# Kernel optimization log

Measured on AMD Instinct MI355X. Metric: run time of the kernel, lower is better.

The kernel has to match this reference:

```python
import jax, jax.numpy as jnp
import numpy as np

IN_DIM = 18 * 2 * 1 * 536  # 19296
H = 512
OUT = 11
STEPS = 1024


def setup_inputs() -> dict:
    key = jax.random.key(0)
    ks = jax.random.split(key, 14)
    s = 0.02  # small init scale for stable LSTM dynamics
    f32 = jnp.float32
    return {
        "inputs": jax.random.normal(ks[0], (STEPS, IN_DIM), dtype=f32),
        "W_in": jax.random.normal(ks[1], (H, IN_DIM), dtype=f32) * s,
        "b_in": jnp.zeros((H,), dtype=f32),
        "Wih0": jax.random.normal(ks[2], (4 * H, H), dtype=f32) * s,
        "Whh0": jax.random.normal(ks[3], (4 * H, H), dtype=f32) * s,
        "bih0": jnp.zeros((4 * H,), dtype=f32),
        "bhh0": jnp.zeros((4 * H,), dtype=f32),
        "Wih1": jax.random.normal(ks[4], (4 * H, H), dtype=f32) * s,
        "Whh1": jax.random.normal(ks[5], (4 * H, H), dtype=f32) * s,
        "bih1": jnp.zeros((4 * H,), dtype=f32),
        "bhh1": jnp.zeros((4 * H,), dtype=f32),
        "W_out": jax.random.normal(ks[6], (OUT, H), dtype=f32) * s,
        "b_out": jnp.zeros((OUT,), dtype=f32),
    }


def _lstm_cell(gates, c):
    # PyTorch gate order: input, forget, cell(g), output
    i, f, g, o = jnp.split(gates, 4, axis=-1)
    c_new = jax.nn.sigmoid(f) * c + jax.nn.sigmoid(i) * jnp.tanh(g)
    h_new = jax.nn.sigmoid(o) * jnp.tanh(c_new)
    return h_new, c_new


def reference(inputs, W_in, b_in, Wih0, Whh0, bih0, bhh0,
              Wih1, Whh1, bih1, bhh1, W_out, b_out):
    # Input projection is time-independent -> batch it across all steps.
    x_proj = inputs @ W_in.T + b_in            # (STEPS, H)
    gx0 = x_proj @ Wih0.T + bih0               # (STEPS, 4H) precomputed layer-0 input gates

    def step(carry, gx0_t):
        h0, c0, h1, c1 = carry
        h0, c0 = _lstm_cell(gx0_t + h0 @ Whh0.T + bhh0, c0)
        h1, c1 = _lstm_cell(h0 @ Wih1.T + bih1 + h1 @ Whh1.T + bhh1, c1)
        return (h0, c0, h1, c1), h1

    z = jnp.zeros((H,), dtype=inputs.dtype)
    (h0, c0, h1, c1), hs = jax.lax.scan(step, (z, z, z, z), gx0)
    outputs = (hs @ W_out.T + b_out)[:, None, :]   # (STEPS, 1, OUT) == torch (steps, batch=1, 11)
    hn = jnp.stack([h0, h1])[:, None, :]           # (num_layers=2, batch=1, H)
    cn = jnp.stack([c0, c1])[:, None, :]
    return outputs, hn, cn
```

## Files before the change

kernel.cpp:

```cpp
#include <hip/hip_runtime.h>
#include <math.h>

typedef unsigned long long ull;
typedef unsigned int u32;
typedef unsigned short u16;
typedef _Float16 half2v __attribute__((ext_vector_type(2)));
typedef __bf16 bf16x8 __attribute__((ext_vector_type(8)));
typedef float f32x4 __attribute__((ext_vector_type(4)));

#define H 512
#define STEPS 1024
#define OUTN 11

__device__ __forceinline__ float sigm(float x) { return 1.f / (1.f + __expf(-x)); }
__device__ __forceinline__ ull ld_pair(const ull* p) {
  return __hip_atomic_load((ull*)p, __ATOMIC_RELAXED, __HIP_MEMORY_SCOPE_AGENT);
}
__device__ __forceinline__ void st_pair(ull* p, ull v) {
  __hip_atomic_store(p, v, __ATOMIC_RELAXED, __HIP_MEMORY_SCOPE_AGENT);
}
__device__ __forceinline__ float dot2acc(half2v a, half2v b, float c) {
#if __has_builtin(__builtin_amdgcn_fdot2)
  return __builtin_amdgcn_fdot2(a, b, c, false);
#else
  return c + (float)a.x * (float)b.x + (float)a.y * (float)b.y;
#endif
}
__device__ __forceinline__ u16 f16bits(float x) {
  return __builtin_bit_cast(u16, (_Float16)x);
}
__device__ __forceinline__ half2v bch2(u32 u) { return __builtin_bit_cast(half2v, u); }

__device__ __forceinline__ u32 split_bf16(float x) {
  u32 u = __float_as_uint(x);
  u32 rh = (u + 0x7FFFu + ((u >> 16) & 1u)) & 0xFFFF0000u;
  float hf = __uint_as_float(rh);
  float lo = x - hf;
  u32 ul = __float_as_uint(lo);
  u32 rl = (ul + 0x7FFFu + ((ul >> 16) & 1u)) & 0xFFFF0000u;
  return (rh >> 16) | rl;
}

__global__ void cvt_split(float* __restrict__ A, float* __restrict__ B, int nA, int n4) {
  int idx = blockIdx.x * 256 + threadIdx.x;
  if (idx >= n4) return;
  int base = idx * 4;
  float* p = (base < nA) ? (A + base) : (B + (base - nA));
  float4 v = *(float4*)p;
  u32 r0 = split_bf16(v.x), r1 = split_bf16(v.y), r2 = split_bf16(v.z), r3 = split_bf16(v.w);
  uint4 o = make_uint4(r0, r1, r2, r3);
  *(uint4*)p = o;
}

__global__ __launch_bounds__(256, 2)
void gemm_hilo(const u32* __restrict__ A2, const u32* __restrict__ B2,
               float* __restrict__ C, int M, int N, int K)
{
  __shared__ __align__(16) u16 Ah[64 * 32], Al[64 * 32], Bh[64 * 32], Bl[64 * 32];
  const int z = blockIdx.z;
  const int zstart = z * 151;
  const int nsteps = (z < 3) ? 151 : 150;
  const int mt = blockIdx.x * 64, nt = blockIdx.y * 64;
  const int tid = threadIdx.x;
  const int row = tid >> 2, cg = (tid & 3) * 8;
  const int wave = tid >> 6, lane = tid & 63;
  const int wm = (wave & 1) * 32, wn = (wave >> 1) * 32;
  const int quad = lane >> 4, l16 = lane & 15;

  f32x4 acc[2][2];
#pragma unroll
  for (int i = 0; i < 2; ++i)
#pragma unroll
    for (int j = 0; j < 2; ++j) acc[i][j] = (f32x4)0.f;

  for (int s = 0; s < nsteps; ++s) {
    const int kb = (zstart + s) * 32;
    {
      const u32* ap = A2 + (size_t)(mt + row) * K + kb + cg;
      const u32* bp = B2 + (size_t)(nt + row) * K + kb + cg;
      uint4 a0 = *(const uint4*)ap, a1 = *(const uint4*)(ap + 4);
      uint4 b0 = *(const uint4*)bp, b1 = *(const uint4*)(bp + 4);
      uint4 hi, lo;
      hi = make_uint4((a0.x & 0xFFFF) | (a0.y << 16), (a0.z & 0xFFFF) | (a0.w << 16),
                      (a1.x & 0xFFFF) | (a1.y << 16), (a1.z & 0xFFFF) | (a1.w << 16));
      lo = make_uint4((a0.x >> 16) | (a0.y & 0xFFFF0000u), (a0.z >> 16) | (a0.w & 0xFFFF0000u),
                      (a1.x >> 16) | (a1.y & 0xFFFF0000u), (a1.z >> 16) | (a1.w & 0xFFFF0000u));
      *(uint4*)&Ah[row * 32 + cg] = hi;
      *(uint4*)&Al[row * 32 + cg] = lo;
      hi = make_uint4((b0.x & 0xFFFF) | (b0.y << 16), (b0.z & 0xFFFF) | (b0.w << 16),
                      (b1.x & 0xFFFF) | (b1.y << 16), (b1.z & 0xFFFF) | (b1.w << 16));
      lo = make_uint4((b0.x >> 16) | (b0.y & 0xFFFF0000u), (b0.z >> 16) | (b0.w & 0xFFFF0000u),
                      (b1.x >> 16) | (b1.y & 0xFFFF0000u), (b1.z >> 16) | (b1.w & 0xFFFF0000u));
      *(uint4*)&Bh[row * 32 + cg] = hi;
      *(uint4*)&Bl[row * 32 + cg] = lo;
    }
    __syncthreads();
    bf16x8 ah[2], al[2], bh[2], bl[2];
#pragma unroll
    for (int mf = 0; mf < 2; ++mf) {
      int r = (wm + mf * 16 + l16) * 32 + quad * 8;
      ah[mf] = *reinterpret_cast<const bf16x8*>(&Ah[r]);
      al[mf] = *reinterpret_cast<const bf16x8*>(&Al[r]);
    }
#pragma unroll
    for (int nf = 0; nf < 2; ++nf) {
      int r = (wn + nf * 16 + l16) * 32 + quad * 8;
      bh[nf] = *reinterpret_cast<const bf16x8*>(&Bh[r]);
      bl[nf] = *reinterpret_cast<const bf16x8*>(&Bl[r]);
    }
#pragma unroll
    for (int mf = 0; mf < 2; ++mf)
#pragma unroll
      for (int nf = 0; nf < 2; ++nf) {
        acc[mf][nf] = __builtin_amdgcn_mfma_f32_16x16x32_bf16(ah[mf], bh[nf], acc[mf][nf], 0, 0, 0);
        acc[mf][nf] = __builtin_amdgcn_mfma_f32_16x16x32_bf16(ah[mf], bl[nf], acc[mf][nf], 0, 0, 0);
        acc[mf][nf] = __builtin_amdgcn_mfma_f32_16x16x32_bf16(al[mf], bh[nf], acc[mf][nf], 0, 0, 0);
      }
    __syncthreads();
  }

#pragma unroll
  for (int mf = 0; mf < 2; ++mf)
#pragma unroll
    for (int nf = 0; nf < 2; ++nf)
#pragma unroll
      for (int r = 0; r < 4; ++r) {
        int rw = mt + wm + mf * 16 + quad * 4 + r;
        int cl = nt + wn + nf * 16 + l16;
        atomicAdd(&C[(size_t)rw * N + cl], acc[mf][nf][r]);
      }
}

#define GBM 64
#define GBN 64
#define GBK 64
#define GLD 76

__global__ __launch_bounds__(256, 2)
void gemm_nt(const float* __restrict__ A, const float* __restrict__ B,
             float* __restrict__ C, const float* __restrict__ bias,
             int M, int N, int K)
{
  __shared__ float As[GBM][GLD];
  __shared__ float Bs[GBN][GLD];
  const int mt = blockIdx.x, nt = blockIdx.y;
  const int tid = threadIdx.x;
  const int tx = tid & 15, ty = tid >> 4;

  float acc[4][4] = {{0.f}};

  for (int kb = 0; kb < K; kb += GBK) {
#pragma unroll
    for (int i = 0; i < 4; ++i) {
      int r = ty + i * 16;
      int gk = kb + tx * 4;
      *(float4*)&As[r][tx * 4] = *(const float4*)(A + (size_t)(mt * GBM + r) * K + gk);
      *(float4*)&Bs[r][tx * 4] = *(const float4*)(B + (size_t)(nt * GBN + r) * K + gk);
    }
    __syncthreads();
#pragma unroll
    for (int k4 = 0; k4 < GBK; k4 += 4) {
      float4 a[4], b[4];
#pragma unroll
      for (int i = 0; i < 4; ++i) a[i] = *(const float4*)&As[ty * 4 + i][k4];
#pragma unroll
      for (int j = 0; j < 4; ++j) b[j] = *(const float4*)&Bs[tx * 4 + j][k4];
#pragma unroll
      for (int i = 0; i < 4; ++i)
#pragma unroll
        for (int j = 0; j < 4; ++j) {
          acc[i][j] = fmaf(a[i].x, b[j].x, acc[i][j]);
          acc[i][j] = fmaf(a[i].y, b[j].y, acc[i][j]);
          acc[i][j] = fmaf(a[i].z, b[j].z, acc[i][j]);
          acc[i][j] = fmaf(a[i].w, b[j].w, acc[i][j]);
        }
    }
    __syncthreads();
  }

#pragma unroll
  for (int i = 0; i < 4; ++i) {
    int m = mt * GBM + ty * 4 + i;
#pragma unroll
    for (int j = 0; j < 4; ++j) {
      int n = nt * GBN + tx * 4 + j;
      C[(size_t)m * N + n] = acc[i][j] + bias[n];
    }
  }
}

__global__ void init_xproj(float* __restrict__ xp, const float* __restrict__ b_in) {
  int i = blockIdx.x * 256 + threadIdx.x;
  xp[i] = b_in[i & (H - 1)];
}

__global__ void out_proj(const float* __restrict__ hs1, const float* __restrict__ Wout,
                         const float* __restrict__ bout, float* __restrict__ out) {
  int idx = blockIdx.x * 256 + threadIdx.x;
  if (idx >= STEPS * OUTN) return;
  int t = idx / OUTN, o = idx - t * OUTN;
  const float* h = hs1 + t * H;
  const float* wr = Wout + o * H;
  float acc = 0.f;
#pragma unroll 4
  for (int i = 0; i < H; i += 4) {
    float4 hv = *(const float4*)(h + i);
    float4 wv = *(const float4*)(wr + i);
    acc = fmaf(hv.x, wv.x, acc);
    acc = fmaf(hv.y, wv.y, acc);
    acc = fmaf(hv.z, wv.z, acc);
    acc = fmaf(hv.w, wv.w, acc);
  }
  out[idx] = acc + bout[o];
}

#define NC0 24
#define NC1 16
#define RD 8

__global__ __launch_bounds__(512, 1)
void lstm_chains(const float* __restrict__ gx0,
                 const float* __restrict__ Whh0, const float* __restrict__ bhh0,
                 const float* __restrict__ Wih1, const float* __restrict__ Whh1,
                 const float* __restrict__ bih1, const float* __restrict__ bhh1,
                 float* __restrict__ hs1, float* __restrict__ out,
                 ull* __restrict__ mb0, ull* __restrict__ mb1,
                 int* __restrict__ flags1)
{
  const int wg = blockIdx.x;
  const int tid = threadIdx.x;
  const bool role0 = (wg < 8);

  __shared__ __align__(16) u32 hl_u[512];
  __shared__ __align__(16) float gbuf[256];
  __shared__ __align__(16) float gxb[256];

  half2v wgt[8][16];
  float bias[8];
  int rg, ch;

  if (role0) {
    rg = tid >> 4; ch = tid & 15;
    int g = rg >> 3, lub = (rg & 7) * 8;
    int growb = (g << 9) + (wg << 6) + lub;
    const float* wb = Whh0 + (size_t)growb * H + ch * 32;
#pragma unroll
    for (int r = 0; r < 8; ++r) {
      const float* wr = wb + (size_t)r * H;
#pragma unroll
      for (int j4 = 0; j4 < 8; ++j4) {
        float4 f = *(const float4*)(wr + j4 * 4);
        wgt[r][2 * j4]     = half2v{(_Float16)f.x, (_Float16)f.y};
        wgt[r][2 * j4 + 1] = half2v{(_Float16)f.z, (_Float16)f.w};
      }
      bias[r] = bhh0[growb + r];
    }
  } else {
    rg = tid >> 5; ch = tid & 31;
    int g = rg >> 2, lub = (rg & 3) * 8;
    int growb = (g << 9) + ((wg - 8) << 5) + lub;
    const float* wb = (ch < 16) ? (Whh1 + (size_t)growb * H + ch * 32)
                                : (Wih1 + (size_t)growb * H + (ch - 16) * 32);
#pragma unroll
    for (int r = 0; r < 8; ++r) {
      const float* wr = wb + (size_t)r * H;
#pragma unroll
      for (int j4 = 0; j4 < 8; ++j4) {
        float4 f = *(const float4*)(wr + j4 * 4);
        wgt[r][2 * j4]     = half2v{(_Float16)f.x, (_Float16)f.y};
        wgt[r][2 * j4 + 1] = half2v{(_Float16)f.z, (_Float16)f.w};
      }
      bias[r] = bih1[growb + r] + bhh1[growb + r];
    }
  }

  float c_state = 0.f, h_last = 0.f;

  if (role0) {
    const int w = wg;
    for (int t = 0; t < STEPS; ++t) {
      if (tid >= 256) {
        int j = tid - 256;
        gxb[j] = gx0[t * 2048 + ((j >> 6) << 9) + (w << 6) + (j & 63)];
        if (j < 16 && (t & 3) == 0 && t > 0) {
          int need = t - 4, f;
          do {
            f = __hip_atomic_load(&flags1[j], __ATOMIC_RELAXED, __HIP_MEMORY_SCOPE_AGENT);
          } while (f < need);
        }
      } else {
        const ull* src = mb0 + ((((w << 3) | ((t + RD - 1) & (RD - 1)))) << 8) + tid;
        ull p;
        do { p = ld_pair(src); } while ((unsigned)(p >> 32) != (unsigned)t);
        hl_u[tid] = (u32)p;
      }
      __syncthreads();

      float accv[8];
#pragma unroll
      for (int r = 0; r < 8; ++r) accv[r] = 0.f;
      {
        const u32* hp = hl_u + (ch << 4);
        uint4 q0 = *(const uint4*)hp;
        uint4 q1 = *(const uint4*)(hp + 4);
        uint4 q2 = *(const uint4*)(hp + 8);
        uint4 q3 = *(const uint4*)(hp + 12);
        half2v h2[16] = {bch2(q0.x), bch2(q0.y), bch2(q0.z), bch2(q0.w),
                         bch2(q1.x), bch2(q1.y), bch2(q1.z), bch2(q1.w),
                         bch2(q2.x), bch2(q2.y), bch2(q2.z), bch2(q2.w),
                         bch2(q3.x), bch2(q3.y), bch2(q3.z), bch2(q3.w)};
#pragma unroll
        for (int j = 0; j < 16; ++j)
#pragma unroll
          for (int r = 0; r < 8; ++r)
            accv[r] = dot2acc(wgt[r][j], h2[j], accv[r]);
      }
#pragma unroll
      for (int o = 1; o < 16; o <<= 1)
#pragma unroll
        for (int r = 0; r < 8; ++r)
          accv[r] += __shfl_xor(accv[r], o);
      if (ch == 0) {
        float4 ga = *(const float4*)&gxb[rg * 8];
        float4 gb = *(const float4*)&gxb[rg * 8 + 4];
        float4 o0 = make_float4(accv[0] + bias[0] + ga.x, accv[1] + bias[1] + ga.y,
                                accv[2] + bias[2] + ga.z, accv[3] + bias[3] + ga.w);
        float4 o1 = make_float4(accv[4] + bias[4] + gb.x, accv[5] + bias[5] + gb.y,
                                accv[6] + bias[6] + gb.z, accv[7] + bias[7] + gb.w);
        *(float4*)&gbuf[rg * 8] = o0;
        *(float4*)&gbuf[rg * 8 + 4] = o1;
      }
      __syncthreads();

      if (tid < 64) {
        float gi = gbuf[tid], gf = gbuf[64 + tid], gg = gbuf[128 + tid], go = gbuf[192 + tid];
        c_state = sigm(gf) * c_state + sigm(gi) * tanhf(gg);
        float hv = sigm(go) * tanhf(c_state);
        float hnb = __shfl_down(hv, 1);
        if ((tid & 1) == 0) {
          u32 payl = (u32)f16bits(hv) | ((u32)f16bits(hnb) << 16);
          ull pay = ((ull)(unsigned)(t + 1) << 32) | (ull)payl;
          const int slot = t & (RD - 1);
          const int pidx = (w << 5) + (tid >> 1);
#pragma unroll
          for (int c = 0; c < NC0; ++c)
            st_pair(mb0 + (((c << 3) | slot) << 8) + pidx, pay);
        }
        h_last = hv;
      }
    }
  } else {
    const int v = wg - 8;
    for (int tau = 1; tau <= STEPS; ++tau) {
      const int t = tau - 1;
      if (tid < 256) {
        const ull* q1 = mb1 + ((((v << 3) | ((t + RD - 1) & (RD - 1)))) << 8) + tid;
        ull p;
        do { p = ld_pair(q1); } while ((unsigned)(p >> 32) != (unsigned)t);
        hl_u[tid] = (u32)p;
      } else {
        const ull* q0 = mb0 + (((((8 + v) << 3) | (t & (RD - 1)))) << 8) + (tid - 256);
        ull p;
        do { p = ld_pair(q0); } while ((unsigned)(p >> 32) != (unsigned)(t + 1));
        hl_u[tid] = (u32)p;
      }
      __syncthreads();

      float accv[8];
#pragma unroll
      for (int r = 0; r < 8; ++r) accv[r] = 0.f;
      {
        const u32* hp = hl_u + (ch << 4);
        uint4 q0 = *(const uint4*)hp;
        uint4 q1 = *(const uint4*)(hp + 4);
        uint4 q2 = *(const uint4*)(hp + 8);
        uint4 q3 = *(const uint4*)(hp + 12);
        half2v h2[16] = {bch2(q0.x), bch2(q0.y), bch2(q0.z), bch2(q0.w),
                         bch2(q1.x), bch2(q1.y), bch2(q1.z), bch2(q1.w),
                         bch2(q2.x), bch2(q2.y), bch2(q2.z), bch2(q2.w),
                         bch2(q3.x), bch2(q3.y), bch2(q3.z), bch2(q3.w)};
#pragma unroll
        for (int j = 0; j < 16; ++j)
#pragma unroll
          for (int r = 0; r < 8; ++r)
            accv[r] = dot2acc(wgt[r][j], h2[j], accv[r]);
      }
#pragma unroll
      for (int o = 1; o < 32; o <<= 1)
#pragma unroll
        for (int r = 0; r < 8; ++r)
          accv[r] += __shfl_xor(accv[r], o);
      if (ch == 0) {
        float4 o0 = make_float4(accv[0] + bias[0], accv[1] + bias[1],
                                accv[2] + bias[2], accv[3] + bias[3]);
        float4 o1 = make_float4(accv[4] + bias[4], accv[5] + bias[5],
                                accv[6] + bias[6], accv[7] + bias[7]);
        *(float4*)&gbuf[rg * 8] = o0;
        *(float4*)&gbuf[rg * 8 + 4] = o1;
      }
      __syncthreads();

      if (tid < 32) {
        int u = (v << 5) + tid;
        float gi = gbuf[tid], gf = gbuf[32 + tid], gg = gbuf[64 + tid], go = gbuf[96 + tid];
        c_state = sigm(gf) * c_state + sigm(gi) * tanhf(gg);
        float hv = sigm(go) * tanhf(c_state);
        float hnb = __shfl_down(hv, 1);
        if ((tid & 1) == 0) {
          u32 payl = (u32)f16bits(hv) | ((u32)f16bits(hnb) << 16);
          ull pay = ((ull)(unsigned)(t + 1) << 32) | (ull)payl;
          const int slot = t & (RD - 1);
          const int pidx = (v << 4) + (tid >> 1);
#pragma unroll
          for (int c = 0; c < NC1; ++c)
            st_pair(mb1 + (((c << 3) | slot) << 8) + pidx, pay);
        }
        h_last = hv;
        hs1[t * H + u] = hv;
      }
      if (tid == 0)
        __hip_atomic_store(&flags1[v], tau, __ATOMIC_RELAXED, __HIP_MEMORY_SCOPE_AGENT);
    }
  }

  if (role0) {
    if (tid < 64) {
      int u = (wg << 6) + tid;
      out[STEPS * OUTN + u] = h_last;
      out[STEPS * OUTN + 2 * H + u] = c_state;
    }
  } else {
    if (tid < 32) {
      int u = ((wg - 8) << 5) + tid;
      out[STEPS * OUTN + H + u] = h_last;
      out[STEPS * OUTN + 3 * H + u] = c_state;
    }
  }
}

extern "C" void kernel_launch(void* const* d_in, const int* in_sizes, int n_in,
                              void* d_out, int out_size, void* d_ws, size_t ws_size,
                              hipStream_t stream)
{
  (void)in_sizes; (void)n_in; (void)out_size; (void)ws_size;
  float* inputs = (float*)d_in[0];
  float* W_in   = (float*)d_in[1];
  const float* b_in   = (const float*)d_in[2];
  const float* Wih0   = (const float*)d_in[3];
  const float* Whh0   = (const float*)d_in[4];
  const float* bih0   = (const float*)d_in[5];
  const float* bhh0   = (const float*)d_in[6];
  const float* Wih1   = (const float*)d_in[7];
  const float* Whh1   = (const float*)d_in[8];
  const float* bih1   = (const float*)d_in[9];
  const float* bhh1   = (const float*)d_in[10];
  const float* W_out  = (const float*)d_in[11];
  const float* b_out  = (const float*)d_in[12];
  float* out = (float*)d_out;
  float* ws = (float*)d_ws;

  float* xp  = ws;
  float* gx0 = ws + 524288;
  float* hs1 = ws + 524288 + 2097152;
  char* syncb = (char*)(ws + 3145728);
  ull* mb0 = (ull*)syncb;
  ull* mb1 = (ull*)(syncb + 24 * 8 * 256 * 8);
  int* flags1 = (int*)(syncb + (24 + 16) * 8 * 256 * 8);

  hipMemsetAsync(syncb, 0, (24 + 16) * 8 * 256 * 8 + 64, stream);

  {
    const int nA = STEPS * 19296;
    const int n4 = (nA + H * 19296) / 4;
    cvt_split<<<n4 / 256, 256, 0, stream>>>(inputs, W_in, nA, n4);
  }
  init_xproj<<<2048, 256, 0, stream>>>(xp, b_in);
  {
    dim3 g(16, 8, 4);
    gemm_hilo<<<g, 256, 0, stream>>>((const u32*)inputs, (const u32*)W_in, xp,
                                     1024, 512, 19296);
  }
  {
    dim3 g(16, 32, 1);
    gemm_nt<<<g, 256, 0, stream>>>(xp, Wih0, gx0, bih0, 1024, 2048, 512);
  }
  lstm_chains<<<24, 512, 0, stream>>>(gx0, Whh0, bhh0, Wih1, Whh1, bih1, bhh1,
                                      hs1, out, mb0, mb1, flags1);
  out_proj<<<44, 256, 0, stream>>>(hs1, W_out, b_out, out);
}
```

Baseline: 3.261 ms.

## Replicate LSTM chains per XCD with local mailboxes and lighter polling

Launches 8 independent replicas of the 24-workgroup recurrent pipeline, grouped by blockIdx modulo 8. This relies on the assumption that the dispatcher places each replica on a single XCD, so that step-to-step handoffs stay in that XCD's L2. Each producer now writes one mailbox entry instead of fanning out 24 or 16 copies, and consumers poll with sc0 inline-asm loads, falling back periodically to an agent-scope atomic load. The layer-1 progress flags are now published only every 4 steps and padded to separate addresses. The cost is 8x redundant compute and duplicated, though identical, output writes, plus a dependence on the hardware workgroup-to-XCD mapping for the locality benefit.

Result: slower. 3.462 ms (+6.2%).

```diff
diff --git a/kernel.cpp b/kernel.cpp
--- a/kernel.cpp
+++ b/kernel.cpp
@@ -13,12 +13,25 @@
 #define OUTN 11
 
 __device__ __forceinline__ float sigm(float x) { return 1.f / (1.f + __expf(-x)); }
-__device__ __forceinline__ ull ld_pair(const ull* p) {
-  return __hip_atomic_load((ull*)p, __ATOMIC_RELAXED, __HIP_MEMORY_SCOPE_AGENT);
-}
-__device__ __forceinline__ void st_pair(ull* p, ull v) {
+
+__device__ __forceinline__ void push_pair(ull* p, ull v) {
   __hip_atomic_store(p, v, __ATOMIC_RELAXED, __HIP_MEMORY_SCOPE_AGENT);
-}
+  asm volatile("global_store_dwordx2 %0, %1, off" :: "v"(p), "v"(v) : "memory");
+}
+__device__ __forceinline__ ull poll_pair(const ull* p, unsigned want) {
+  for (;;) {
+#pragma unroll 1
+    for (int s = 0; s < 8; ++s) {
+      ull r;
+      asm volatile("global_load_dwordx2 %0, %1, off sc0\n\ts_waitcnt vmcnt(0)"
+                   : "=&v"(r) : "v"(p) : "memory");
+      if ((unsigned)(r >> 32) == want) return r;
+    }
+    ull r = __hip_atomic_load((ull*)p, __ATOMIC_RELAXED, __HIP_MEMORY_SCOPE_AGENT);
+    if ((unsigned)(r >> 32) == want) return r;
+  }
+}
+
 __device__ __forceinline__ float dot2acc(half2v a, half2v b, float c) {
 #if __has_builtin(__builtin_amdgcn_fdot2)
   return __builtin_amdgcn_fdot2(a, b, c, false);
@@ -214,9 +227,9 @@
   out[idx] = acc + bout[o];
 }
 
-#define NC0 24
-#define NC1 16
 #define RD 8
+#define NGRP 8
+#define GSZ_ULL 8192
 
 __global__ __launch_bounds__(512, 1)
 void lstm_chains(const float* __restrict__ gx0,
@@ -224,12 +237,17 @@
                  const float* __restrict__ Wih1, const float* __restrict__ Whh1,
                  const float* __restrict__ bih1, const float* __restrict__ bhh1,
                  float* __restrict__ hs1, float* __restrict__ out,
-                 ull* __restrict__ mb0, ull* __restrict__ mb1,
-                 int* __restrict__ flags1)
+                 ull* __restrict__ mbase)
 {
-  const int wg = blockIdx.x;
+  const int bid = blockIdx.x;
+  const int grp = bid & 7;
+  const int wg  = bid >> 3;
   const int tid = threadIdx.x;
   const bool role0 = (wg < 8);
+
+  ull* mb0 = mbase + (size_t)grp * GSZ_ULL;
+  ull* mb1 = mb0 + 2048;
+  int* flg = (int*)(mb0 + 4096);
 
   __shared__ __align__(16) u32 hl_u[512];
   __shared__ __align__(16) float gbuf[256];
@@ -284,14 +302,14 @@
         gxb[j] = gx0[t * 2048 + ((j >> 6) << 9) + (w << 6) + (j & 63)];
         if (j < 16 && (t & 3) == 0 && t > 0) {
           int need = t - 4, f;
+          const int* fp = flg + (j << 4);
           do {
-            f = __hip_atomic_load(&flags1[j], __ATOMIC_RELAXED, __HIP_MEMORY_SCOPE_AGENT);
+            f = __hip_atomic_load((int*)fp, __ATOMIC_RELAXED, __HIP_MEMORY_SCOPE_AGENT);
           } while (f < need);
         }
       } else {
-        const ull* src = mb0 + ((((w << 3) | ((t + RD - 1) & (RD - 1)))) << 8) + tid;
-        ull p;
-        do { p = ld_pair(src); } while ((unsigned)(p >> 32) != (unsigned)t);
+        const ull* src = mb0 + (((t + RD - 1) & (RD - 1)) << 8) + tid;
+        ull p = poll_pair(src, (unsigned)t);
         hl_u[tid] = (u32)p;
       }
       __syncthreads();
@@ -342,9 +360,7 @@
           ull pay = ((ull)(unsigned)(t + 1) << 32) | (ull)payl;
           const int slot = t & (RD - 1);
           const int pidx = (w << 5) + (tid >> 1);
-#pragma unroll
-          for (int c = 0; c < NC0; ++c)
-            st_pair(mb0 + (((c << 3) | slot) << 8) + pidx, pay);
+          push_pair(mb0 + (slot << 8) + pidx, pay);
         }
         h_last = hv;
       }
@@ -354,14 +370,12 @@
     for (int tau = 1; tau <= STEPS; ++tau) {
       const int t = tau - 1;
       if (tid < 256) {
-        const ull* q1 = mb1 + ((((v << 3) | ((t + RD - 1) & (RD - 1)))) << 8) + tid;
-        ull p;
-        do { p = ld_pair(q1); } while ((unsigned)(p >> 32) != (unsigned)t);
+        const ull* q1 = mb1 + (((t + RD - 1) & (RD - 1)) << 8) + tid;
+        ull p = poll_pair(q1, (unsigned)t);
         hl_u[tid] = (u32)p;
       } else {
-        const ull* q0 = mb0 + (((((8 + v) << 3) | (t & (RD - 1)))) << 8) + (tid - 256);
-        ull p;
-        do { p = ld_pair(q0); } while ((unsigned)(p >> 32) != (unsigned)(t + 1));
+        const ull* q0 = mb0 + ((t & (RD - 1)) << 8) + (tid - 256);
+        ull p = poll_pair(q0, (unsigned)(t + 1));
         hl_u[tid] = (u32)p;
       }
       __syncthreads();
@@ -411,15 +425,13 @@
           ull pay = ((ull)(unsigned)(t + 1) << 32) | (ull)payl;
           const int slot = t & (RD - 1);
           const int pidx = (v << 4) + (tid >> 1);
-#pragma unroll
-          for (int c = 0; c < NC1; ++c)
-            st_pair(mb1 + (((c << 3) | slot) << 8) + pidx, pay);
+          push_pair(mb1 + (slot << 8) + pidx, pay);
         }
         h_last = hv;
         hs1[t * H + u] = hv;
       }
-      if (tid == 0)
-        __hip_atomic_store(&flags1[v], tau, __ATOMIC_RELAXED, __HIP_MEMORY_SCOPE_AGENT);
+      if (((tau & 3) == 0) && tid == 64)
+        __hip_atomic_store(flg + (v << 4), tau, __ATOMIC_RELAXED, __HIP_MEMORY_SCOPE_AGENT);
     }
   }
 
@@ -463,11 +475,9 @@
   float* gx0 = ws + 524288;
   float* hs1 = ws + 524288 + 2097152;
   char* syncb = (char*)(ws + 3145728);
-  ull* mb0 = (ull*)syncb;
-  ull* mb1 = (ull*)(syncb + 24 * 8 * 256 * 8);
-  int* flags1 = (int*)(syncb + (24 + 16) * 8 * 256 * 8);
-
-  hipMemsetAsync(syncb, 0, (24 + 16) * 8 * 256 * 8 + 64, stream);
+  ull* mbase = (ull*)syncb;
+
+  hipMemsetAsync(syncb, 0, NGRP * GSZ_ULL * 8, stream);
 
   {
     const int nA = STEPS * 19296;
@@ -484,7 +494,7 @@
     dim3 g(16, 32, 1);
     gemm_nt<<<g, 256, 0, stream>>>(xp, Wih0, gx0, bih0, 1024, 2048, 512);
   }
-  lstm_chains<<<24, 512, 0, stream>>>(gx0, Whh0, bhh0, Wih1, Whh1, bih1, bhh1,
-                                      hs1, out, mb0, mb1, flags1);
+  lstm_chains<<<192, 512, 0, stream>>>(gx0, Whh0, bhh0, Wih1, Whh1, bih1, bhh1,
+                                       hs1, out, mbase);
   out_proj<<<44, 256, 0, stream>>>(hs1, W_out, b_out, out);
 }
```
